# Kernel optimization log

Hardware: AMD Instinct MI355X
Metric: run time of the kernel (lower is better)

## Reference

```python
import jax, jax.numpy as jnp
import numpy as np

N = 50000      # nodes in the block
M = 10         # mailbox_size
H = 8          # attention heads
DIN = 128      # dim_in (per-mail message dim)
DOUT = 128     # dim_out (memory dim)
DT = 128       # dim_time
LN_EPS = 1e-5
LRELU_SLOPE = 0.2


def setup_inputs() -> dict:
    key = jax.random.key(0)
    ks = jax.random.split(key, 16)
    s = 0.05  # small init scale for weights
    return {
        # forward tensor args
        "mem": jax.random.normal(ks[0], (N, DOUT), jnp.float32),
        "mem_input": jax.random.normal(ks[1], (N, M * DIN), jnp.float32),
        "ts": jax.random.uniform(ks[2], (N,), jnp.float32) * 100.0,
        "mail_ts": jax.random.uniform(ks[3], (N, M), jnp.float32) * 100.0,
        # learned parameters (torch Linear convention: W is [out, in])
        "wq_w": jax.random.normal(ks[4], (DOUT, DOUT), jnp.float32) * s,
        "wq_b": jnp.zeros((DOUT,), jnp.float32),
        "wk_w": jax.random.normal(ks[5], (DOUT, DIN + DT), jnp.float32) * s,
        "wk_b": jnp.zeros((DOUT,), jnp.float32),
        "wv_w": jax.random.normal(ks[6], (DOUT, DIN + DT), jnp.float32) * s,
        "wv_b": jnp.zeros((DOUT,), jnp.float32),
        "ln_g": jnp.ones((DOUT,), jnp.float32),
        "ln_b": jnp.zeros((DOUT,), jnp.float32),
        "mlp_w": jax.random.normal(ks[7], (DOUT, DOUT), jnp.float32) * s,
        "mlp_b": jnp.zeros((DOUT,), jnp.float32),
        # TimeEncode: cos(dt * te_w + te_b), te_w = 1/10^linspace(0,9,DT) as in TGN
        "te_w": (1.0 / (10.0 ** np.linspace(0, 9, DT))).astype(np.float32),
        "te_b": jnp.zeros((DT,), jnp.float32),
    }


def reference(mem, mem_input, ts, mail_ts,
              wq_w, wq_b, wk_w, wk_b, wv_w, wv_b,
              ln_g, ln_b, mlp_w, mlp_b, te_w, te_b):
    n = mem.shape[0]
    # Q: [n, H, Dh]
    Q = (mem @ wq_w.T + wq_b).reshape(n, H, -1)
    # mails: [n, M, DIN]
    mails = mem_input.reshape(n, M, -1)
    # time encoding of (src ts - mail ts): [n, M, DT]
    dt = ts[:, None] - mail_ts
    time_feat = jnp.cos(dt[:, :, None] * te_w + te_b)
    mails = jnp.concatenate([mails, time_feat], axis=2)  # [n, M, DIN+DT]
    K = (mails @ wk_w.T + wk_b).reshape(n, M, H, -1)
    V = (mails @ wv_w.T + wv_b).reshape(n, M, H, -1)
    # elementwise QK reduction over head dim, LeakyReLU, softmax over mailbox
    att = jnp.einsum('nhd,nmhd->nmh', Q, K)
    att = jax.nn.leaky_relu(att, LRELU_SLOPE)
    att = jax.nn.softmax(att, axis=1)          # (att_dropout = identity in eval)
    rst = jnp.einsum('nmh,nmhd->nhd', att, V).reshape(n, -1)
    rst = rst + mem                             # residual
    # LayerNorm
    mu = rst.mean(axis=-1, keepdims=True)
    var = ((rst - mu) ** 2).mean(axis=-1, keepdims=True)
    rst = (rst - mu) / jnp.sqrt(var + LN_EPS) * ln_g + ln_b
    # MLP + (dropout = identity in eval) + ReLU
    rst = rst @ mlp_w.T + mlp_b
    return jax.nn.relu(rst)
```

## Files before the change

### kernel.cpp

```cpp
#include <hip/hip_runtime.h>
#include <hip/hip_bf16.h>

#define N_NODES 50000
#define NB 32
#define LN_EPS 1e-5f
#define SLOPE 0.2f

typedef __attribute__((ext_vector_type(8))) short bf16x8;
typedef __attribute__((ext_vector_type(4))) float f32x4;

__device__ __forceinline__ int imin(int a, int b){ return a < b ? a : b; }

__device__ __forceinline__ short f2bf(float f){
  union { float f; unsigned u; } v; v.f = f;
  unsigned r = v.u + 0x7fffu + ((v.u >> 16) & 1u);
  return (short)(r >> 16);
}

__device__ __forceinline__ float rsum16_dpp(float x){
  asm volatile(
    "s_nop 1\n\t"
    "v_add_f32_dpp %0, %0, %0 row_ror:8 row_mask:0xf bank_mask:0xf\n\t"
    "s_nop 1\n\t"
    "v_add_f32_dpp %0, %0, %0 row_ror:4 row_mask:0xf bank_mask:0xf\n\t"
    "s_nop 1\n\t"
    "v_add_f32_dpp %0, %0, %0 row_ror:2 row_mask:0xf bank_mask:0xf\n\t"
    "s_nop 1\n\t"
    "v_add_f32_dpp %0, %0, %0 row_ror:1 row_mask:0xf bank_mask:0xf"
    : "+v"(x));
  return x;
}

__device__ __forceinline__ unsigned cvtpk(float a, float b){
  unsigned r;
  asm("v_cvt_pk_bf16_f32 %0, %1, %2" : "=v"(r) : "v"(a), "v"(b));
  return r;
}

__device__ __forceinline__ bf16x8 pack8(float4 a, float4 b){
  union { unsigned u[4]; bf16x8 v; } r;
  r.u[0] = cvtpk(a.x, a.y); r.u[1] = cvtpk(a.z, a.w);
  r.u[2] = cvtpk(b.x, b.y); r.u[3] = cvtpk(b.z, b.w);
  return r.v;
}

#define WKP 0
#define WVP 32768
#define WQP 65536
#define MLPP 81920

__global__ __launch_bounds__(256) void prep_pack(
    const float* __restrict__ wq, const float* __restrict__ wk,
    const float* __restrict__ wv, const float* __restrict__ mlp,
    unsigned short* __restrict__ wsP)
{
  int idx = blockIdx.x * 256 + threadIdx.x;
  const float* src; int base, K, local;
  if (idx < 32768)      { src = wk;  base = WKP;  local = idx;         K = 256; }
  else if (idx < 65536) { src = wv;  base = WVP;  local = idx - 32768; K = 256; }
  else if (idx < 81920) { src = wq;  base = WQP;  local = idx - 65536; K = 128; }
  else if (idx < 98304) { src = mlp; base = MLPP; local = idx - 81920; K = 128; }
  else return;
  int i  = local & 7;
  int l  = (local >> 3) & 63;
  int nt = (local >> 9) & 7;
  int ks = local >> 12;
  int row = nt * 16 + (l & 15);
  int k   = ks * 32 + ((l >> 4) << 3) + i;
  wsP[base + local] = (unsigned short)f2bf(src[row * K + k]);
}

__device__ __forceinline__ void stage_write(
    unsigned short* sAp, const float* sTs, const float* sMts,
    const float* sTeW, const float* sTeB,
    float4 f0, float4 f1, float4 f2, float4 f3,
    int srow, int skc, int ssw, int g0, int m)
{
  float dt = sTs[srow] - sMts[srow*10 + m];
  const float4* tw = (const float4*)(sTeW + skc);
  const float4* tb = (const float4*)(sTeB + skc);
  float4 w0 = tw[0], w1 = tw[1], w2 = tw[2], w3 = tw[3];
  float4 b0 = tb[0], b1 = tb[1], b2 = tb[2], b3 = tb[3];
  float4 c0, c1, c2, c3;
  c0.x=__cosf(dt*w0.x+b0.x); c0.y=__cosf(dt*w0.y+b0.y); c0.z=__cosf(dt*w0.z+b0.z); c0.w=__cosf(dt*w0.w+b0.w);
  c1.x=__cosf(dt*w1.x+b1.x); c1.y=__cosf(dt*w1.y+b1.y); c1.z=__cosf(dt*w1.z+b1.z); c1.w=__cosf(dt*w1.w+b1.w);
  c2.x=__cosf(dt*w2.x+b2.x); c2.y=__cosf(dt*w2.y+b2.y); c2.z=__cosf(dt*w2.z+b2.z); c2.w=__cosf(dt*w2.w+b2.w);
  c3.x=__cosf(dt*w3.x+b3.x); c3.y=__cosf(dt*w3.y+b3.y); c3.z=__cosf(dt*w3.z+b3.z); c3.w=__cosf(dt*w3.w+b3.w);
  bf16x8* dst = (bf16x8*)sAp;
  dst[srow*32 + ((g0     ) ^ ssw)] = pack8(f0, f1);
  dst[srow*32 + ((g0 + 1 ) ^ ssw)] = pack8(f2, f3);
  dst[srow*32 + ((16 + g0) ^ ssw)] = pack8(c0, c1);
  dst[srow*32 + ((17 + g0) ^ ssw)] = pack8(c2, c3);
}

__global__ __launch_bounds__(256, 2) void fused_tmu(
    const float* __restrict__ mem, const float* __restrict__ mem_input,
    const float* __restrict__ ts, const float* __restrict__ mail_ts,
    const float* __restrict__ wq_b, const float* __restrict__ wk_b,
    const float* __restrict__ wv_b, const float* __restrict__ ln_g,
    const float* __restrict__ ln_b, const float* __restrict__ mlp_b,
    const float* __restrict__ te_w, const float* __restrict__ te_b,
    const unsigned short* __restrict__ wsP, float* __restrict__ out)
{
  __shared__ __align__(16) unsigned short sA[2 * NB * 256];
  __shared__ float sTs[NB];
  __shared__ float sMts[NB * 10];
  __shared__ float sTeW[128], sTeB[128];
  __shared__ float sRed[NB * 8];

  const int tid  = threadIdx.x;
  const int lane = tid & 63;
  const int wid  = tid >> 6;
  const int l15  = lane & 15;
  const int lg   = lane >> 4;
  const int h0   = wid * 2;
  const int node0 = blockIdx.x * NB;

  const int srow = tid >> 3;
  const int skc  = (tid & 7) << 4;
  const int sgn  = imin(node0 + srow, N_NODES - 1);
  const int ssw  = srow & 7;
  const int g0   = skc >> 3;
  const float* miBase = mem_input + (size_t)sgn * 1280 + skc;

  float4 fm0, fm1, fm2, fm3, fa0, fa1, fa2, fa3;
  {
    const float4* mp = (const float4*)(mem + (size_t)sgn * 128 + skc);
    fm0 = mp[0]; fm1 = mp[1]; fm2 = mp[2]; fm3 = mp[3];
    const float4* mi0 = (const float4*)(miBase);
    fa0 = mi0[0]; fa1 = mi0[1]; fa2 = mi0[2]; fa3 = mi0[3];
  }

  if (tid < NB) sTs[tid] = ts[imin(node0 + tid, N_NODES - 1)];
  if (tid < 128){ sTeW[tid] = te_w[tid]; sTeB[tid] = te_b[tid]; }
  {
    int idx = tid;
    int nn = idx / 10, mm = idx - nn * 10;
    sMts[idx] = mail_ts[(size_t)imin(node0 + nn, N_NODES - 1) * 10 + mm];
    idx = tid + 256;
    if (idx < NB * 10){
      nn = idx / 10; mm = idx - nn * 10;
      sMts[idx] = mail_ts[(size_t)imin(node0 + nn, N_NODES - 1) * 10 + mm];
    }
  }
  {
    bf16x8* dst = (bf16x8*)sA;
    dst[NB*32 + srow*32 + ((g0    ) ^ ssw)] = pack8(fm0, fm1);
    dst[NB*32 + srow*32 + ((g0 + 1) ^ ssw)] = pack8(fm2, fm3);
  }

  float qb[2], kb[2], vb[2];
  #pragma unroll
  for (int hh = 0; hh < 2; hh++){
    int c = (h0 + hh) * 16 + l15;
    qb[hh] = wq_b[c]; kb[hh] = wk_b[c]; vb[hh] = wv_b[c];
  }

  const bf16x8* wsv = (const bf16x8*)wsP;
  bf16x8 wqf[4][2];
  #pragma unroll
  for (int ks = 0; ks < 4; ks++)
    #pragma unroll
    for (int hh = 0; hh < 2; hh++)
      wqf[ks][hh] = wsv[WQP/8 + (ks*8 + h0 + hh)*64 + lane];

  __syncthreads();

  f32x4 z4 = {0.f, 0.f, 0.f, 0.f};
  f32x4 qac[2][2];
  #pragma unroll
  for (int ntr = 0; ntr < 2; ntr++)
    #pragma unroll
    for (int hh = 0; hh < 2; hh++)
      qac[ntr][hh] = (f32x4){qb[hh], qb[hh], qb[hh], qb[hh]};
  {
    const bf16x8* P1 = (const bf16x8*)sA + NB*32;
    #pragma unroll
    for (int ntr = 0; ntr < 2; ntr++){
      int r = ntr*16 + l15, rs = r & 7;
      #pragma unroll
      for (int ks = 0; ks < 4; ks++){
        bf16x8 af = P1[r*32 + ((ks*4 + lg) ^ rs)];
        qac[ntr][0] = __builtin_amdgcn_mfma_f32_16x16x32_bf16(af, wqf[ks][0], qac[ntr][0], 0, 0, 0);
        qac[ntr][1] = __builtin_amdgcn_mfma_f32_16x16x32_bf16(af, wqf[ks][1], qac[ntr][1], 0, 0, 0);
      }
    }
  }

  stage_write(sA, sTs, sMts, sTeW, sTeB, fa0, fa1, fa2, fa3, srow, skc, ssw, g0, 0);
  {
    const float4* mi1 = (const float4*)(miBase + 128);
    fa0 = mi1[0]; fa1 = mi1[1]; fa2 = mi1[2]; fa3 = mi1[3];
  }

  bf16x8 wkf[8][2], wvf[8][2];
  #pragma unroll
  for (int ks = 0; ks < 8; ks++)
    #pragma unroll
    for (int hh = 0; hh < 2; hh++){
      wkf[ks][hh] = wsv[WKP/8 + (ks*8 + h0 + hh)*64 + lane];
      wvf[ks][hh] = wsv[WVP/8 + (ks*8 + h0 + hh)*64 + lane];
    }

  __syncthreads();

  f32x4 pv[2][2] = {{z4, z4}, {z4, z4}};
  f32x4 sm[2][2] = {{z4, z4}, {z4, z4}};
  for (int m = 0; m < 10; m++){
    const bf16x8* P = (const bf16x8*)sA + (m & 1) * NB*32;
    #pragma unroll
    for (int ntr = 0; ntr < 2; ntr++){
      int r = ntr*16 + l15, rs = r & 7;
      f32x4 ka[2] = {z4, z4}, va[2] = {z4, z4};
      #pragma unroll
      for (int ks = 0; ks < 8; ks++){
        bf16x8 af = P[r*32 + ((ks*4 + lg) ^ rs)];
        ka[0] = __builtin_amdgcn_mfma_f32_16x16x32_bf16(af, wkf[ks][0], ka[0], 0, 0, 0);
        ka[1] = __builtin_amdgcn_mfma_f32_16x16x32_bf16(af, wkf[ks][1], ka[1], 0, 0, 0);
        va[0] = __builtin_amdgcn_mfma_f32_16x16x32_bf16(af, wvf[ks][0], va[0], 0, 0, 0);
        va[1] = __builtin_amdgcn_mfma_f32_16x16x32_bf16(af, wvf[ks][1], va[1], 0, 0, 0);
      }
      #pragma unroll
      for (int hh = 0; hh < 2; hh++){
        #pragma unroll
        for (int j = 0; j < 4; j++){
          float lv = (ka[hh][j] + kb[hh]) * qac[ntr][hh][j];
          lv = rsum16_dpp(lv);
          lv = fmaxf(lv, SLOPE * lv);
          lv = fminf(lv, 60.f);
          float p = __expf(lv);
          sm[ntr][hh][j] += p;
          pv[ntr][hh][j] += p * va[hh][j];
        }
      }
    }
    if (m < 9){
      stage_write(sA + ((m+1) & 1) * NB*256, sTs, sMts, sTeW, sTeB,
                  fa0, fa1, fa2, fa3, srow, skc, ssw, g0, m+1);
      if (m < 8){
        const float4* mi = (const float4*)(miBase + (size_t)(m+2)*128);
        fa0 = mi[0]; fa1 = mi[1]; fa2 = mi[2]; fa3 = mi[3];
      }
    }
    __syncthreads();
  }

  float lgv[2], lbv[2], mbv[2];
  #pragma unroll
  for (int hh = 0; hh < 2; hh++){
    int c = (h0 + hh) * 16 + l15;
    lgv[hh] = ln_g[c]; lbv[hh] = ln_b[c]; mbv[hh] = mlp_b[c];
  }
  float rstv[2][2][4];
  #pragma unroll
  for (int ntr = 0; ntr < 2; ntr++)
    #pragma unroll
    for (int hh = 0; hh < 2; hh++)
      #pragma unroll
      for (int j = 0; j < 4; j++){
        float o = pv[ntr][hh][j] / sm[ntr][hh][j] + vb[hh];
        int gn = imin(node0 + ntr*16 + lg*4 + j, N_NODES - 1);
        rstv[ntr][hh][j] = o + mem[(size_t)gn * 128 + (h0 + hh)*16 + l15];
      }
  #pragma unroll
  for (int ntr = 0; ntr < 2; ntr++)
    #pragma unroll
    for (int j = 0; j < 4; j++){
      float s = rstv[ntr][0][j] + rstv[ntr][1][j];
      float q = rstv[ntr][0][j]*rstv[ntr][0][j] + rstv[ntr][1][j]*rstv[ntr][1][j];
      s = rsum16_dpp(s); q = rsum16_dpp(q);
      if (l15 == 0){
        int nl = ntr*16 + lg*4 + j;
        sRed[nl*8 + wid*2    ] = s;
        sRed[nl*8 + wid*2 + 1] = q;
      }
    }
  __syncthreads();
  #pragma unroll
  for (int ntr = 0; ntr < 2; ntr++)
    #pragma unroll
    for (int hh = 0; hh < 2; hh++)
      #pragma unroll
      for (int j = 0; j < 4; j++){
        int nl = ntr*16 + lg*4 + j;
        float sum = sRed[nl*8] + sRed[nl*8+2] + sRed[nl*8+4] + sRed[nl*8+6];
        float sq  = sRed[nl*8+1] + sRed[nl*8+3] + sRed[nl*8+5] + sRed[nl*8+7];
        float mu  = sum * (1.f/128.f);
        float var = sq * (1.f/128.f) - mu*mu;
        float rs  = rsqrtf(var + LN_EPS);
        float y = (rstv[ntr][hh][j] - mu) * rs * lgv[hh] + lbv[hh];
        int c = (h0 + hh)*16 + l15;
        sA[nl*256 + ((c >> 3) ^ (nl & 7))*8 + (c & 7)] = (unsigned short)f2bf(y);
      }

  bf16x8 mlpf[4][2];
  #pragma unroll
  for (int ks = 0; ks < 4; ks++)
    #pragma unroll
    for (int hh = 0; hh < 2; hh++)
      mlpf[ks][hh] = wsv[MLPP/8 + (ks*8 + h0 + hh)*64 + lane];
  __syncthreads();

  f32x4 mac[2][2];
  #pragma unroll
  for (int ntr = 0; ntr < 2; ntr++)
    #pragma unroll
    for (int hh = 0; hh < 2; hh++)
      mac[ntr][hh] = (f32x4){mbv[hh], mbv[hh], mbv[hh], mbv[hh]};
  {
    const bf16x8* P0 = (const bf16x8*)sA;
    #pragma unroll
    for (int ntr = 0; ntr < 2; ntr++){
      int r = ntr*16 + l15, rs = r & 7;
      #pragma unroll
      for (int ks = 0; ks < 4; ks++){
        bf16x8 af = P0[r*32 + ((ks*4 + lg) ^ rs)];
        mac[ntr][0] = __builtin_amdgcn_mfma_f32_16x16x32_bf16(af, mlpf[ks][0], mac[ntr][0], 0, 0, 0);
        mac[ntr][1] = __builtin_amdgcn_mfma_f32_16x16x32_bf16(af, mlpf[ks][1], mac[ntr][1], 0, 0, 0);
      }
    }
  }
  #pragma unroll
  for (int ntr = 0; ntr < 2; ntr++)
    #pragma unroll
    for (int hh = 0; hh < 2; hh++)
      #pragma unroll
      for (int j = 0; j < 4; j++){
        float o = fmaxf(mac[ntr][hh][j], 0.f);
        int node = node0 + ntr*16 + lg*4 + j;
        if (node < N_NODES)
          out[(size_t)node * 128 + (h0 + hh)*16 + l15] = o;
      }
}

extern "C" void kernel_launch(void* const* d_in, const int* in_sizes, int n_in,
                              void* d_out, int out_size, void* d_ws, size_t ws_size,
                              hipStream_t stream)
{
  const float* mem       = (const float*)d_in[0];
  const float* mem_input = (const float*)d_in[1];
  const float* ts        = (const float*)d_in[2];
  const float* mail_ts   = (const float*)d_in[3];
  const float* wq_w      = (const float*)d_in[4];
  const float* wq_b      = (const float*)d_in[5];
  const float* wk_w      = (const float*)d_in[6];
  const float* wk_b      = (const float*)d_in[7];
  const float* wv_w      = (const float*)d_in[8];
  const float* wv_b      = (const float*)d_in[9];
  const float* ln_g      = (const float*)d_in[10];
  const float* ln_b      = (const float*)d_in[11];
  const float* mlp_w     = (const float*)d_in[12];
  const float* mlp_b     = (const float*)d_in[13];
  const float* te_w      = (const float*)d_in[14];
  const float* te_b      = (const float*)d_in[15];
  unsigned short* wsP = (unsigned short*)d_ws;
  float* outp = (float*)d_out;

  prep_pack<<<384, 256, 0, stream>>>(wq_w, wk_w, wv_w, mlp_w, wsP);
  int nblk = (N_NODES + NB - 1) / NB;
  fused_tmu<<<nblk, 256, 0, stream>>>(mem, mem_input, ts, mail_ts,
      wq_b, wk_b, wv_b, ln_g, ln_b, mlp_b, te_w, te_b, wsP, outp);
}
```

Measured before the change: 166.1 us.

## Split work across 8 waves, one head per wave, 512-thread blocks

Blocks grow from 256 to 512 threads, so each of 8 waves handles one attention head instead of two. This halves per-thread register fragments (K/V/Q/MLP weights and accumulators) and staging loads, and raises launch bounds to 4 blocks per SM for more waves in flight. The LayerNorm cross-wave reduction grows to 8 partials per node. The Q projection is also reordered after the first mail staging write. The trade-off is more waves sharing the same LDS tile and more barrier participants per block, and the higher launch bound may force register spills.

```diff
diff --git a/kernel.cpp b/kernel.cpp
--- a/kernel.cpp
+++ b/kernel.cpp
@@ -73,27 +73,22 @@
 __device__ __forceinline__ void stage_write(
     unsigned short* sAp, const float* sTs, const float* sMts,
     const float* sTeW, const float* sTeB,
-    float4 f0, float4 f1, float4 f2, float4 f3,
-    int srow, int skc, int ssw, int g0, int m)
+    float4 f0, float4 f1, int srow, int skc, int ssw, int sg, int m)
 {
   float dt = sTs[srow] - sMts[srow*10 + m];
   const float4* tw = (const float4*)(sTeW + skc);
   const float4* tb = (const float4*)(sTeB + skc);
-  float4 w0 = tw[0], w1 = tw[1], w2 = tw[2], w3 = tw[3];
-  float4 b0 = tb[0], b1 = tb[1], b2 = tb[2], b3 = tb[3];
-  float4 c0, c1, c2, c3;
+  float4 w0 = tw[0], w1 = tw[1];
+  float4 b0 = tb[0], b1 = tb[1];
+  float4 c0, c1;
   c0.x=__cosf(dt*w0.x+b0.x); c0.y=__cosf(dt*w0.y+b0.y); c0.z=__cosf(dt*w0.z+b0.z); c0.w=__cosf(dt*w0.w+b0.w);
   c1.x=__cosf(dt*w1.x+b1.x); c1.y=__cosf(dt*w1.y+b1.y); c1.z=__cosf(dt*w1.z+b1.z); c1.w=__cosf(dt*w1.w+b1.w);
-  c2.x=__cosf(dt*w2.x+b2.x); c2.y=__cosf(dt*w2.y+b2.y); c2.z=__cosf(dt*w2.z+b2.z); c2.w=__cosf(dt*w2.w+b2.w);
-  c3.x=__cosf(dt*w3.x+b3.x); c3.y=__cosf(dt*w3.y+b3.y); c3.z=__cosf(dt*w3.z+b3.z); c3.w=__cosf(dt*w3.w+b3.w);
   bf16x8* dst = (bf16x8*)sAp;
-  dst[srow*32 + ((g0     ) ^ ssw)] = pack8(f0, f1);
-  dst[srow*32 + ((g0 + 1 ) ^ ssw)] = pack8(f2, f3);
-  dst[srow*32 + ((16 + g0) ^ ssw)] = pack8(c0, c1);
-  dst[srow*32 + ((17 + g0) ^ ssw)] = pack8(c2, c3);
-}
-
-__global__ __launch_bounds__(256, 2) void fused_tmu(
+  dst[srow*32 + (sg ^ ssw)]      = pack8(f0, f1);
+  dst[srow*32 + 16 + (sg ^ ssw)] = pack8(c0, c1);
+}
+
+__global__ __launch_bounds__(512, 4) void fused_tmu(
     const float* __restrict__ mem, const float* __restrict__ mem_input,
     const float* __restrict__ ts, const float* __restrict__ mail_ts,
     const float* __restrict__ wq_b, const float* __restrict__ wk_b,
@@ -106,73 +101,59 @@
   __shared__ float sTs[NB];
   __shared__ float sMts[NB * 10];
   __shared__ float sTeW[128], sTeB[128];
-  __shared__ float sRed[NB * 8];
+  __shared__ float sRed[NB * 16];
 
   const int tid  = threadIdx.x;
   const int lane = tid & 63;
   const int wid  = tid >> 6;
   const int l15  = lane & 15;
   const int lg   = lane >> 4;
-  const int h0   = wid * 2;
   const int node0 = blockIdx.x * NB;
 
-  const int srow = tid >> 3;
-  const int skc  = (tid & 7) << 4;
+  const int srow = tid >> 4;
+  const int sg   = tid & 15;
+  const int skc  = sg << 3;
   const int sgn  = imin(node0 + srow, N_NODES - 1);
   const int ssw  = srow & 7;
-  const int g0   = skc >> 3;
   const float* miBase = mem_input + (size_t)sgn * 1280 + skc;
 
-  float4 fm0, fm1, fm2, fm3, fa0, fa1, fa2, fa3;
+  float4 fm0, fm1, fa0, fa1;
   {
     const float4* mp = (const float4*)(mem + (size_t)sgn * 128 + skc);
-    fm0 = mp[0]; fm1 = mp[1]; fm2 = mp[2]; fm3 = mp[3];
+    fm0 = mp[0]; fm1 = mp[1];
     const float4* mi0 = (const float4*)(miBase);
-    fa0 = mi0[0]; fa1 = mi0[1]; fa2 = mi0[2]; fa3 = mi0[3];
+    fa0 = mi0[0]; fa1 = mi0[1];
   }
 
   if (tid < NB) sTs[tid] = ts[imin(node0 + tid, N_NODES - 1)];
   if (tid < 128){ sTeW[tid] = te_w[tid]; sTeB[tid] = te_b[tid]; }
-  {
-    int idx = tid;
-    int nn = idx / 10, mm = idx - nn * 10;
-    sMts[idx] = mail_ts[(size_t)imin(node0 + nn, N_NODES - 1) * 10 + mm];
-    idx = tid + 256;
-    if (idx < NB * 10){
-      nn = idx / 10; mm = idx - nn * 10;
-      sMts[idx] = mail_ts[(size_t)imin(node0 + nn, N_NODES - 1) * 10 + mm];
-    }
+  if (tid < NB * 10){
+    int nn = tid / 10, mm = tid - nn * 10;
+    sMts[tid] = mail_ts[(size_t)imin(node0 + nn, N_NODES - 1) * 10 + mm];
   }
   {
     bf16x8* dst = (bf16x8*)sA;
-    dst[NB*32 + srow*32 + ((g0    ) ^ ssw)] = pack8(fm0, fm1);
-    dst[NB*32 + srow*32 + ((g0 + 1) ^ ssw)] = pack8(fm2, fm3);
-  }
-
-  float qb[2], kb[2], vb[2];
-  #pragma unroll
-  for (int hh = 0; hh < 2; hh++){
-    int c = (h0 + hh) * 16 + l15;
-    qb[hh] = wq_b[c]; kb[hh] = wk_b[c]; vb[hh] = wv_b[c];
-  }
+    dst[NB*32 + srow*32 + (sg ^ ssw)] = pack8(fm0, fm1);
+  }
+
+  const int c = wid * 16 + l15;
+  float qb = wq_b[c], kb = wk_b[c], vb = wv_b[c];
 
   const bf16x8* wsv = (const bf16x8*)wsP;
-  bf16x8 wqf[4][2];
+  bf16x8 wqf[4];
   #pragma unroll
   for (int ks = 0; ks < 4; ks++)
-    #pragma unroll
-    for (int hh = 0; hh < 2; hh++)
-      wqf[ks][hh] = wsv[WQP/8 + (ks*8 + h0 + hh)*64 + lane];
+    wqf[ks] = wsv[WQP/8 + (ks*8 + wid)*64 + lane];
 
   __syncthreads();
 
+  stage_write(sA, sTs, sMts, sTeW, sTeB, fa0, fa1, srow, skc, ssw, sg, 0);
+  { const float4* mi1 = (const float4*)(miBase + 128); fa0 = mi1[0]; fa1 = mi1[1]; }
+
   f32x4 z4 = {0.f, 0.f, 0.f, 0.f};
-  f32x4 qac[2][2];
-  #pragma unroll
-  for (int ntr = 0; ntr < 2; ntr++)
-    #pragma unroll
-    for (int hh = 0; hh < 2; hh++)
-      qac[ntr][hh] = (f32x4){qb[hh], qb[hh], qb[hh], qb[hh]};
+  f32x4 qac[2];
+  qac[0] = (f32x4){qb, qb, qb, qb};
+  qac[1] = qac[0];
   {
     const bf16x8* P1 = (const bf16x8*)sA + NB*32;
     #pragma unroll
@@ -181,132 +162,105 @@
       #pragma unroll
       for (int ks = 0; ks < 4; ks++){
         bf16x8 af = P1[r*32 + ((ks*4 + lg) ^ rs)];
-        qac[ntr][0] = __builtin_amdgcn_mfma_f32_16x16x32_bf16(af, wqf[ks][0], qac[ntr][0], 0, 0, 0);
-        qac[ntr][1] = __builtin_amdgcn_mfma_f32_16x16x32_bf16(af, wqf[ks][1], qac[ntr][1], 0, 0, 0);
-      }
-    }
-  }
-
-  stage_write(sA, sTs, sMts, sTeW, sTeB, fa0, fa1, fa2, fa3, srow, skc, ssw, g0, 0);
-  {
-    const float4* mi1 = (const float4*)(miBase + 128);
-    fa0 = mi1[0]; fa1 = mi1[1]; fa2 = mi1[2]; fa3 = mi1[3];
-  }
-
-  bf16x8 wkf[8][2], wvf[8][2];
-  #pragma unroll
-  for (int ks = 0; ks < 8; ks++)
-    #pragma unroll
-    for (int hh = 0; hh < 2; hh++){
-      wkf[ks][hh] = wsv[WKP/8 + (ks*8 + h0 + hh)*64 + lane];
-      wvf[ks][hh] = wsv[WVP/8 + (ks*8 + h0 + hh)*64 + lane];
-    }
+        qac[ntr] = __builtin_amdgcn_mfma_f32_16x16x32_bf16(af, wqf[ks], qac[ntr], 0, 0, 0);
+      }
+    }
+  }
+
+  bf16x8 wkf[8], wvf[8];
+  #pragma unroll
+  for (int ks = 0; ks < 8; ks++){
+    wkf[ks] = wsv[WKP/8 + (ks*8 + wid)*64 + lane];
+    wvf[ks] = wsv[WVP/8 + (ks*8 + wid)*64 + lane];
+  }
 
   __syncthreads();
 
-  f32x4 pv[2][2] = {{z4, z4}, {z4, z4}};
-  f32x4 sm[2][2] = {{z4, z4}, {z4, z4}};
+  f32x4 pv[2] = {z4, z4};
+  f32x4 sm[2] = {z4, z4};
   for (int m = 0; m < 10; m++){
     const bf16x8* P = (const bf16x8*)sA + (m & 1) * NB*32;
     #pragma unroll
     for (int ntr = 0; ntr < 2; ntr++){
       int r = ntr*16 + l15, rs = r & 7;
-      f32x4 ka[2] = {z4, z4}, va[2] = {z4, z4};
+      f32x4 ka = z4, va = z4;
       #pragma unroll
       for (int ks = 0; ks < 8; ks++){
         bf16x8 af = P[r*32 + ((ks*4 + lg) ^ rs)];
-        ka[0] = __builtin_amdgcn_mfma_f32_16x16x32_bf16(af, wkf[ks][0], ka[0], 0, 0, 0);
-        ka[1] = __builtin_amdgcn_mfma_f32_16x16x32_bf16(af, wkf[ks][1], ka[1], 0, 0, 0);
-        va[0] = __builtin_amdgcn_mfma_f32_16x16x32_bf16(af, wvf[ks][0], va[0], 0, 0, 0);
-        va[1] = __builtin_amdgcn_mfma_f32_16x16x32_bf16(af, wvf[ks][1], va[1], 0, 0, 0);
-      }
-      #pragma unroll
-      for (int hh = 0; hh < 2; hh++){
-        #pragma unroll
-        for (int j = 0; j < 4; j++){
-          float lv = (ka[hh][j] + kb[hh]) * qac[ntr][hh][j];
-          lv = rsum16_dpp(lv);
-          lv = fmaxf(lv, SLOPE * lv);
-          lv = fminf(lv, 60.f);
-          float p = __expf(lv);
-          sm[ntr][hh][j] += p;
-          pv[ntr][hh][j] += p * va[hh][j];
-        }
+        ka = __builtin_amdgcn_mfma_f32_16x16x32_bf16(af, wkf[ks], ka, 0, 0, 0);
+        va = __builtin_amdgcn_mfma_f32_16x16x32_bf16(af, wvf[ks], va, 0, 0, 0);
+      }
+      #pragma unroll
+      for (int j = 0; j < 4; j++){
+        float lv = (ka[j] + kb) * qac[ntr][j];
+        lv = rsum16_dpp(lv);
+        lv = fmaxf(lv, SLOPE * lv);
+        lv = fminf(lv, 60.f);
+        float p = __expf(lv);
+        sm[ntr][j] += p;
+        pv[ntr][j] += p * va[j];
       }
     }
     if (m < 9){
       stage_write(sA + ((m+1) & 1) * NB*256, sTs, sMts, sTeW, sTeB,
-                  fa0, fa1, fa2, fa3, srow, skc, ssw, g0, m+1);
+                  fa0, fa1, srow, skc, ssw, sg, m+1);
       if (m < 8){
         const float4* mi = (const float4*)(miBase + (size_t)(m+2)*128);
-        fa0 = mi[0]; fa1 = mi[1]; fa2 = mi[2]; fa3 = mi[3];
+        fa0 = mi[0]; fa1 = mi[1];
       }
     }
     __syncthreads();
   }
 
-  float lgv[2], lbv[2], mbv[2];
-  #pragma unroll
-  for (int hh = 0; hh < 2; hh++){
-    int c = (h0 + hh) * 16 + l15;
-    lgv[hh] = ln_g[c]; lbv[hh] = ln_b[c]; mbv[hh] = mlp_b[c];
-  }
-  float rstv[2][2][4];
+  float lgv = ln_g[c], lbv = ln_b[c], mbv = mlp_b[c];
+  float rstv[2][4];
   #pragma unroll
   for (int ntr = 0; ntr < 2; ntr++)
     #pragma unroll
-    for (int hh = 0; hh < 2; hh++)
-      #pragma unroll
-      for (int j = 0; j < 4; j++){
-        float o = pv[ntr][hh][j] / sm[ntr][hh][j] + vb[hh];
-        int gn = imin(node0 + ntr*16 + lg*4 + j, N_NODES - 1);
-        rstv[ntr][hh][j] = o + mem[(size_t)gn * 128 + (h0 + hh)*16 + l15];
-      }
+    for (int j = 0; j < 4; j++){
+      int gn = imin(node0 + ntr*16 + lg*4 + j, N_NODES - 1);
+      rstv[ntr][j] = pv[ntr][j] / sm[ntr][j] + vb + mem[(size_t)gn * 128 + c];
+    }
   #pragma unroll
   for (int ntr = 0; ntr < 2; ntr++)
     #pragma unroll
     for (int j = 0; j < 4; j++){
-      float s = rstv[ntr][0][j] + rstv[ntr][1][j];
-      float q = rstv[ntr][0][j]*rstv[ntr][0][j] + rstv[ntr][1][j]*rstv[ntr][1][j];
-      s = rsum16_dpp(s); q = rsum16_dpp(q);
+      float s = rsum16_dpp(rstv[ntr][j]);
+      float q = rsum16_dpp(rstv[ntr][j] * rstv[ntr][j]);
       if (l15 == 0){
         int nl = ntr*16 + lg*4 + j;
-        sRed[nl*8 + wid*2    ] = s;
-        sRed[nl*8 + wid*2 + 1] = q;
+        sRed[nl*16 + wid*2    ] = s;
+        sRed[nl*16 + wid*2 + 1] = q;
       }
     }
   __syncthreads();
   #pragma unroll
   for (int ntr = 0; ntr < 2; ntr++)
     #pragma unroll
-    for (int hh = 0; hh < 2; hh++)
-      #pragma unroll
-      for (int j = 0; j < 4; j++){
-        int nl = ntr*16 + lg*4 + j;
-        float sum = sRed[nl*8] + sRed[nl*8+2] + sRed[nl*8+4] + sRed[nl*8+6];
-        float sq  = sRed[nl*8+1] + sRed[nl*8+3] + sRed[nl*8+5] + sRed[nl*8+7];
-        float mu  = sum * (1.f/128.f);
-        float var = sq * (1.f/128.f) - mu*mu;
-        float rs  = rsqrtf(var + LN_EPS);
-        float y = (rstv[ntr][hh][j] - mu) * rs * lgv[hh] + lbv[hh];
-        int c = (h0 + hh)*16 + l15;
-        sA[nl*256 + ((c >> 3) ^ (nl & 7))*8 + (c & 7)] = (unsigned short)f2bf(y);
-      }
-
-  bf16x8 mlpf[4][2];
+    for (int j = 0; j < 4; j++){
+      int nl = ntr*16 + lg*4 + j;
+      float sum = 0.f, sq = 0.f;
+      #pragma unroll
+      for (int w = 0; w < 8; w++){
+        sum += sRed[nl*16 + w*2];
+        sq  += sRed[nl*16 + w*2 + 1];
+      }
+      float mu  = sum * (1.f/128.f);
+      float var = sq * (1.f/128.f) - mu*mu;
+      float rs  = rsqrtf(var + LN_EPS);
+      float y = (rstv[ntr][j] - mu) * rs * lgv + lbv;
+      sA[nl*256 + ((c >> 3) ^ (nl & 7))*8 + (c & 7)] = (unsigned short)f2bf(y);
+    }
+
+  bf16x8 mlpf[4];
   #pragma unroll
   for (int ks = 0; ks < 4; ks++)
-    #pragma unroll
-    for (int hh = 0; hh < 2; hh++)
-      mlpf[ks][hh] = wsv[MLPP/8 + (ks*8 + h0 + hh)*64 + lane];
+    mlpf[ks] = wsv[MLPP/8 + (ks*8 + wid)*64 + lane];
   __syncthreads();
 
-  f32x4 mac[2][2];
-  #pragma unroll
-  for (int ntr = 0; ntr < 2; ntr++)
-    #pragma unroll
-    for (int hh = 0; hh < 2; hh++)
-      mac[ntr][hh] = (f32x4){mbv[hh], mbv[hh], mbv[hh], mbv[hh]};
+  f32x4 mac[2];
+  mac[0] = (f32x4){mbv, mbv, mbv, mbv};
+  mac[1] = mac[0];
   {
     const bf16x8* P0 = (const bf16x8*)sA;
     #pragma unroll
@@ -315,22 +269,19 @@
       #pragma unroll
       for (int ks = 0; ks < 4; ks++){
         bf16x8 af = P0[r*32 + ((ks*4 + lg) ^ rs)];
-        mac[ntr][0] = __builtin_amdgcn_mfma_f32_16x16x32_bf16(af, mlpf[ks][0], mac[ntr][0], 0, 0, 0);
-        mac[ntr][1] = __builtin_amdgcn_mfma_f32_16x16x32_bf16(af, mlpf[ks][1], mac[ntr][1], 0, 0, 0);
+        mac[ntr] = __builtin_amdgcn_mfma_f32_16x16x32_bf16(af, mlpf[ks], mac[ntr], 0, 0, 0);
       }
     }
   }
   #pragma unroll
   for (int ntr = 0; ntr < 2; ntr++)
     #pragma unroll
-    for (int hh = 0; hh < 2; hh++)
-      #pragma unroll
-      for (int j = 0; j < 4; j++){
-        float o = fmaxf(mac[ntr][hh][j], 0.f);
-        int node = node0 + ntr*16 + lg*4 + j;
-        if (node < N_NODES)
-          out[(size_t)node * 128 + (h0 + hh)*16 + l15] = o;
-      }
+    for (int j = 0; j < 4; j++){
+      float o = fmaxf(mac[ntr][j], 0.f);
+      int node = node0 + ntr*16 + lg*4 + j;
+      if (node < N_NODES)
+        out[(size_t)node * 128 + c] = o;
+    }
 }
 
 extern "C" void kernel_launch(void* const* d_in, const int* in_sizes, int n_in,
@@ -358,6 +309,6 @@
 
   prep_pack<<<384, 256, 0, stream>>>(wq_w, wk_w, wv_w, mlp_w, wsP);
   int nblk = (N_NODES + NB - 1) / NB;
-  fused_tmu<<<nblk, 256, 0, stream>>>(mem, mem_input, ts, mail_ts,
+  fused_tmu<<<nblk, 512, 0, stream>>>(mem, mem_input, ts, mail_ts,
       wq_b, wk_b, wv_b, ln_g, ln_b, mlp_b, te_w, te_b, wsP, outp);
 }
```

New measurement: 264.9 us. 59.4% more time.
